# Optimization experiments

Measured on AMD Instinct MI355X. Metric: run time of the kernel, lower is better.

The kernel has to match this reference:

```python
import jax, jax.numpy as jnp
import numpy as np

EPS = 1e-6

def _layernorm2d(x, w, b):
    # normalize over channel dim (axis=1) per (b,h,w)
    u = jnp.mean(x, axis=1, keepdims=True)
    s = jnp.mean((x - u) ** 2, axis=1, keepdims=True)
    xn = (x - u) / jnp.sqrt(s + EPS)
    return xn * w[None, :, None, None] + b[None, :, None, None]

def _conv1x1(x, w, b):
    # w: (O, C, 1, 1)
    y = jnp.einsum('bchw,oc->bohw', x, w[:, :, 0, 0])
    return y + b[None, :, None, None]

def _dwconv3x3(x, w):
    # w: (C, 1, 3, 3), groups = C, padding 1, no bias
    C = x.shape[1]
    return jax.lax.conv_general_dilated(
        x, w, window_strides=(1, 1), padding=((1, 1), (1, 1)),
        dimension_numbers=('NCHW', 'OIHW', 'NCHW'), feature_group_count=C)

def _linrec_scan(a, u, axis):
    # s_t = a_t * s_{t-1} + u_t via associative scan
    def comb(l, r):
        al, ul = l
        ar, ur = r
        return al * ar, ar * ul + ur
    return jax.lax.associative_scan(comb, (a, u), axis=axis)[1]

def _bidir_scan(z, a, b, g, axis):
    u = b * z
    s_f = _linrec_scan(a, u, axis)
    s_b = jnp.flip(_linrec_scan(jnp.flip(a, axis), jnp.flip(u, axis), axis), axis)
    return g * (s_f + s_b)

def setup_inputs() -> dict:
    key = jax.random.key(0)
    ks = jax.random.split(key, 6)
    B, C, H, W = 8, 192, 128, 128
    x = jax.random.normal(ks[0], (B, C, H, W), dtype=jnp.float32)
    ln_w = jnp.ones((C,), jnp.float32)
    ln_b = jnp.zeros((C,), jnp.float32)
    dw_w = jax.random.normal(ks[1], (C, 1, 3, 3), jnp.float32) * (1.0 / 3.0)
    loc_w = jax.random.normal(ks[2], (C, C, 1, 1), jnp.float32) * (1.0 / np.sqrt(C))
    loc_b = jnp.zeros((C,), jnp.float32)
    par_w = jax.random.normal(ks[3], (3 * C, C, 1, 1), jnp.float32) * (1.0 / np.sqrt(C))
    par_b = jnp.zeros((3 * C,), jnp.float32)
    out_w = jax.random.normal(ks[4], (C, C, 1, 1), jnp.float32) * (1.0 / np.sqrt(C))
    out_b = jnp.zeros((C,), jnp.float32)
    return {"x": x, "ln_w": ln_w, "ln_b": ln_b, "dw_w": dw_w,
            "loc_w": loc_w, "loc_b": loc_b, "par_w": par_w, "par_b": par_b,
            "out_w": out_w, "out_b": out_b}

def reference(x, ln_w, ln_b, dw_w, loc_w, loc_b, par_w, par_b, out_w, out_b):
    C = x.shape[1]
    z = _layernorm2d(x, ln_w, ln_b)
    local_feat = _conv1x1(_dwconv3x3(z, dw_w), loc_w, loc_b)
    gates = _conv1x1(z, par_w, par_b)
    alpha = jax.nn.sigmoid(gates[:, :C])
    beta = jax.nn.sigmoid(gates[:, C:2 * C])
    gamma = jax.nn.sigmoid(gates[:, 2 * C:])
    y_w = _bidir_scan(z, alpha, beta, gamma, axis=3)  # along W
    y_h = _bidir_scan(z, alpha, beta, gamma, axis=2)  # along H
    y = local_feat + 0.5 * (y_w + y_h)
    y = jax.nn.silu(y)
    y = _conv1x1(y, out_w, out_b)
    return x + y
```

## Files before the change

### kernel.cpp

```cpp
#include <hip/hip_runtime.h>
#include <cstdint>
#include <cstddef>

#define B 8
#define C 192
#define H 128
#define W 128
#define HW (H * W)
#define CHW ((size_t)C * HW)
#define K C

typedef __attribute__((ext_vector_type(8))) short short8v;
typedef __attribute__((ext_vector_type(4))) float f32x4;
typedef __attribute__((ext_vector_type(4))) unsigned short ushort4v;

__device__ __forceinline__ float bf2f(unsigned short s) {
    union { float f; unsigned u; } cv; cv.u = ((unsigned)s) << 16; return cv.f;
}
__device__ __forceinline__ unsigned short f2bf(float f) {
    union { float f; unsigned u; } cv; cv.f = f;
    unsigned r = (cv.u + 0x7fffu + ((cv.u >> 16) & 1u)) >> 16;
    return (unsigned short)r;
}

__global__ void prepack_kernel(const float* __restrict__ pw, const float* __restrict__ lw,
                               const float* __restrict__ ow, unsigned short* __restrict__ wb) {
    int i = blockIdx.x * 256 + threadIdx.x;
    const int NPW = 3 * C * K, NL = C * K;
    if (i < NPW) wb[i] = f2bf(pw[i]);
    else if (i < NPW + NL) wb[i] = f2bf(lw[i - NPW]);
    else if (i < NPW + 2 * NL) wb[i] = f2bf(ow[i - NPW - NL]);
}

__global__ void ln_kernel(const float* __restrict__ x, const float* __restrict__ lw,
                          const float* __restrict__ lb, unsigned short* __restrict__ zt) {
    int p = blockIdx.x * 256 + threadIdx.x;
    int b = p >> 14, hw = p & 16383;
    const float* xp = x + (size_t)b * CHW + hw;
    float sum = 0.f, sq = 0.f;
    for (int c = 0; c < C; ++c) {
        float v = xp[(size_t)c * HW];
        sum += v; sq += v * v;
    }
    float mean = sum * (1.0f / C);
    float var = fmaxf(sq * (1.0f / C) - mean * mean, 0.f);
    float rs = rsqrtf(var + 1e-6f);
    unsigned short* zp = zt + (size_t)p * K;
#pragma unroll 4
    for (int c8 = 0; c8 < K / 8; ++c8) {
        short8v v;
#pragma unroll
        for (int j = 0; j < 8; ++j) {
            int c = c8 * 8 + j;
            float r = (xp[(size_t)c * HW] - mean) * rs * lw[c] + lb[c];
            v[j] = (short)f2bf(r);
        }
        *(short8v*)(zp + c8 * 8) = v;
    }
}

template <int MODE>
__global__ __launch_bounds__(256, 2)
void conv_mfma_kernel(const unsigned short* __restrict__ zt, const unsigned short* __restrict__ yin,
                      const unsigned short* __restrict__ wb, const float* __restrict__ bias,
                      const float* __restrict__ xres, float* __restrict__ Pf,
                      unsigned short* __restrict__ PA, unsigned short* __restrict__ PU,
                      unsigned short* __restrict__ PG) {
    extern __shared__ char smem[];
    int tid = threadIdx.x;
    int lane = tid & 63, wv = tid >> 6;
    int p0 = blockIdx.x * 256 + wv * 64;
    int lr = lane & 15, lh = lane >> 4;
    int sw = (lr & 7) << 4;

    short8v bfr[4][6];
    if (MODE != 2) {
#pragma unroll
        for (int s = 0; s < 4; ++s) {
            const unsigned short* zr = zt + (size_t)(p0 + s * 16 + lr) * K + lh * 8;
#pragma unroll
            for (int t = 0; t < 6; ++t) bfr[s][t] = *(const short8v*)(zr + t * 32);
        }
    } else {
        int bl = p0 >> 14, hwb = p0 & 16383;
        const unsigned short* yb = yin + (size_t)bl * CHW;
#pragma unroll
        for (int s = 0; s < 4; ++s) {
            int hw = hwb + s * 16 + lr;
#pragma unroll
            for (int t = 0; t < 6; ++t) {
                int c0 = t * 32 + lh * 8;
                short8v v;
#pragma unroll
                for (int j = 0; j < 8; ++j)
                    v[j] = (short)yb[(size_t)(c0 + j) * HW + hw];
                bfr[s][t] = v;
            }
        }
    }

    const int NGY = (MODE == 0) ? 3 : 1;
    for (int gy = 0; gy < NGY; ++gy) {
        if (gy) __syncthreads();
        const unsigned short* wsrc = wb + (size_t)gy * C * K;
#pragma unroll
        for (int it = 0; it < 18; ++it) {
            int e8 = it * 256 + tid;
            int row = e8 / 24;
            int cb = (e8 % 24) * 16;
            short8v v = *(const short8v*)(wsrc + e8 * 8);
            *(short8v*)(smem + row * 384 + (cb ^ ((row & 7) << 4))) = v;
        }
        __syncthreads();

        for (int ot = 0; ot < 12; ++ot) {
            int row = ot * 16 + lr;
            int rb = row * 384;
            f32x4 acc[4];
#pragma unroll
            for (int s = 0; s < 4; ++s) acc[s] = (f32x4){0.f, 0.f, 0.f, 0.f};
#pragma unroll
            for (int t = 0; t < 6; ++t) {
                short8v af = *(const short8v*)(smem + rb + ((t * 64 + lh * 16) ^ sw));
#pragma unroll
                for (int s = 0; s < 4; ++s)
                    acc[s] = __builtin_amdgcn_mfma_f32_16x16x32_bf16(bfr[s][t], af, acc[s], 0, 0, 0);
            }
            int o = row;
            float bi = bias[(MODE == 0 ? gy * C : 0) + o];
#pragma unroll
            for (int s = 0; s < 4; ++s) {
                int pst = p0 + s * 16 + lh * 4;
                int bl = pst >> 14, hw = pst & 16383;
                if (MODE == 0) {
                    ushort4v q;
#pragma unroll
                    for (int j = 0; j < 4; ++j) {
                        float v = acc[s][j] + bi;
                        v = 1.f / (1.f + __expf(-v));
                        if (gy == 1) v *= bf2f(zt[(size_t)(pst + j) * K + o]);
                        q[j] = f2bf(v);
                    }
                    unsigned short* dst = (gy == 0) ? PA : ((gy == 1) ? PU : PG);
                    *(ushort4v*)(dst + (size_t)bl * CHW + (size_t)o * HW + hw) = q;
                } else if (MODE == 1) {
                    ushort4v q;
#pragma unroll
                    for (int j = 0; j < 4; ++j) q[j] = f2bf(acc[s][j] + bi);
                    *(ushort4v*)(PA + (size_t)bl * CHW + (size_t)o * HW + hw) = q;
                } else {
                    size_t ad = (size_t)bl * CHW + (size_t)o * HW + hw;
                    f32x4 x4 = *(const f32x4*)(xres + ad);
                    f32x4 q;
#pragma unroll
                    for (int j = 0; j < 4; ++j) q[j] = acc[s][j] + bi + x4[j];
                    *(f32x4*)(Pf + ad) = q;
                }
            }
        }
    }
}

#define TROWS 180
#define LPAD  392
__global__ __launch_bounds__(256, 2)
void dw3x3_kernel(const unsigned short* __restrict__ zt, const float* __restrict__ wgt,
                  unsigned short* __restrict__ dt) {
    __shared__ char lds[TROWS * LPAD];
    int tid = threadIdx.x;
    int bx = blockIdx.x;
    int bimg = bx >> 7;
    int rem = bx & 127;
    int th = rem >> 3, tw = rem & 7;
    int h0 = th * 8, w0 = tw * 16;
    size_t ibase = (size_t)bimg * HW;

    for (int e = tid; e < TROWS * 24; e += 256) {
        int row = e / 24, ch = e % 24;
        int hh = row / 18, ww = row % 18;
        int h = h0 - 1 + hh, w = w0 - 1 + ww;
        short8v v;
        if (h >= 0 && h < H && w >= 0 && w < W)
            v = *(const short8v*)(zt + (ibase + h * W + w) * K + ch * 8);
        else
            v = (short8v){0, 0, 0, 0, 0, 0, 0, 0};
        *(short8v*)(lds + row * LPAD + ch * 16) = v;
    }
    __syncthreads();

    int w_l = tid & 15, h_l = (tid >> 4) & 7, half = tid >> 7;
    int p_out = (h0 + h_l) * W + (w0 + w_l);
    unsigned short* dp = dt + (ibase + p_out) * K + half * 96;
#pragma unroll
    for (int cc = 0; cc < 12; ++cc) {
        int c8 = half * 12 + cc;
        float acc[8];
#pragma unroll
        for (int j = 0; j < 8; ++j) acc[j] = 0.f;
#pragma unroll
        for (int dy = -1; dy <= 1; ++dy) {
#pragma unroll
            for (int dx = -1; dx <= 1; ++dx) {
                int row = (h_l + 1 + dy) * 18 + (w_l + 1 + dx);
                short8v zv = *(const short8v*)(lds + row * LPAD + c8 * 16);
                int t = (dy + 1) * 3 + (dx + 1);
#pragma unroll
                for (int j = 0; j < 8; ++j)
                    acc[j] += wgt[(c8 * 8 + j) * 9 + t] * bf2f((unsigned short)zv[j]);
            }
        }
        short8v ov;
#pragma unroll
        for (int j = 0; j < 8; ++j) ov[j] = (short)f2bf(acc[j]);
        *(short8v*)(dp + cc * 8) = ov;
    }
}

__global__ __launch_bounds__(1024)
void scan_fused_kernel(const unsigned short* __restrict__ A_, const unsigned short* __restrict__ U_,
                       const unsigned short* __restrict__ G_, unsigned short* __restrict__ LY) {
    extern __shared__ float Sl[];
    float* AF = Sl + HW;
    float* UF = AF + 1024;
    float* AB = UF + 1024;
    float* UB = AB + 1024;
    int tid = threadIdx.x, lane = tid & 63, wvi = tid >> 6;
    size_t pb = (size_t)blockIdx.x * HW;

#pragma unroll
    for (int i = 0; i < 8; ++i) {
        int r = wvi * 8 + i;
        size_t base = pb + (size_t)r * W;
        ushort2 av = *(const ushort2*)(A_ + base + 2 * lane);
        ushort2 uv = *(const ushort2*)(U_ + base + 2 * lane);
        float a0 = bf2f(av.x), a1 = bf2f(av.y);
        float u0 = bf2f(uv.x), u1 = bf2f(uv.y);

        float Aa = a0 * a1;
        float Uu = a1 * u0 + u1;
#pragma unroll
        for (int d = 1; d < 64; d <<= 1) {
            float Ao = __shfl_up(Aa, (unsigned)d, 64);
            float Uo = __shfl_up(Uu, (unsigned)d, 64);
            if (lane >= d) { Uu = Aa * Uo + Uu; Aa = Aa * Ao; }
        }
        float sp = __shfl_up(Uu, 1u, 64);
        if (lane == 0) sp = 0.f;
        float s0 = a0 * sp + u0;
        float s1 = a1 * s0 + u1;

        Aa = a0 * a1;
        Uu = a0 * u1 + u0;
#pragma unroll
        for (int d = 1; d < 64; d <<= 1) {
            float Ao = __shfl_down(Aa, (unsigned)d, 64);
            float Uo = __shfl_down(Uu, (unsigned)d, 64);
            if (lane + d < 64) { Uu = Aa * Uo + Uu; Aa = Aa * Ao; }
        }
        float tn = __shfl_down(Uu, 1u, 64);
        if (lane == 63) tn = 0.f;
        float t1 = a1 * tn + u1;
        float t0 = a0 * t1 + u0;

        Sl[r * W + 2 * lane]     = s0 + t0;
        Sl[r * W + 2 * lane + 1] = s1 + t1;
    }

    int w = tid & 127, ck = tid >> 7;
    int h0 = ck * 16;
    float av[16], uv[16];
#pragma unroll
    for (int i = 0; i < 16; ++i) {
        size_t off = pb + (size_t)(h0 + i) * W + w;
        av[i] = bf2f(A_[off]);
        uv[i] = bf2f(U_[off]);
    }
    float Af = 1.f, Uf = 0.f, Ab = 1.f, Ub = 0.f;
#pragma unroll
    for (int i = 0; i < 16; ++i) { Uf = av[i] * Uf + uv[i]; Af *= av[i]; }
#pragma unroll
    for (int i = 15; i >= 0; --i) { Ub = av[i] * Ub + uv[i]; Ab *= av[i]; }
    AF[ck * 128 + w] = Af; UF[ck * 128 + w] = Uf;
    AB[ck * 128 + w] = Ab; UB[ck * 128 + w] = Ub;
    __syncthreads();

    if (tid < 128) {
        float s = 0.f;
#pragma unroll
        for (int k = 0; k < 8; ++k) {
            float Aa = AF[k * 128 + tid], Uu = UF[k * 128 + tid];
            UF[k * 128 + tid] = s;
            s = Aa * s + Uu;
        }
    } else if (tid < 256) {
        int ww = tid - 128;
        float s = 0.f;
#pragma unroll
        for (int k = 7; k >= 0; --k) {
            float Aa = AB[k * 128 + ww], Uu = UB[k * 128 + ww];
            UB[k * 128 + ww] = s;
            s = Aa * s + Uu;
        }
    }
    __syncthreads();

    float sf = UF[ck * 128 + w];
    float sfa[16];
#pragma unroll
    for (int i = 0; i < 16; ++i) { sf = av[i] * sf + uv[i]; sfa[i] = sf; }
    float sb = UB[ck * 128 + w];
#pragma unroll
    for (int i = 15; i >= 0; --i) {
        sb = av[i] * sb + uv[i];
        size_t off = pb + (size_t)(h0 + i) * W + w;
        float g = bf2f(G_[off]);
        float v = bf2f(LY[off]) + 0.5f * g * (Sl[(h0 + i) * W + w] + sfa[i] + sb);
        LY[off] = f2bf(v / (1.f + __expf(-v)));
    }
}

extern "C" void kernel_launch(void* const* d_in, const int* in_sizes, int n_in,
                              void* d_out, int out_size, void* d_ws, size_t ws_size,
                              hipStream_t stream) {
    const float* x     = (const float*)d_in[0];
    const float* ln_w  = (const float*)d_in[1];
    const float* ln_b  = (const float*)d_in[2];
    const float* dw_w  = (const float*)d_in[3];
    const float* loc_w = (const float*)d_in[4];
    const float* loc_b = (const float*)d_in[5];
    const float* par_w = (const float*)d_in[6];
    const float* par_b = (const float*)d_in[7];
    const float* out_w = (const float*)d_in[8];
    const float* out_b = (const float*)d_in[9];
    float* out = (float*)d_out;
    unsigned short* wsu = (unsigned short*)d_ws;

    const int WBN = 5 * C * K;
    int nb = 8;
    while (nb > 1) {
        size_t need = (size_t)WBN * 2 + (size_t)5 * nb * CHW * 2;
        if (need <= ws_size) break;
        nb >>= 1;
    }

    prepack_kernel<<<(WBN + 255) / 256, 256, 0, stream>>>(par_w, loc_w, out_w, wsu);

    for (int b0 = 0; b0 < B; b0 += nb) {
        size_t ge = (size_t)nb * CHW;
        unsigned short* WB = wsu;
        unsigned short* Ab = wsu + WBN;
        unsigned short* Ub = Ab + ge;
        unsigned short* Gb = Ub + ge;
        unsigned short* ZT = Gb + ge;
        unsigned short* DT = ZT + ge;
        const float* xg = x + (size_t)b0 * CHW;
        int npg = nb * HW;

        ln_kernel<<<npg / 256, 256, 0, stream>>>(xg, ln_w, ln_b, ZT);
        conv_mfma_kernel<0><<<npg / 256, 256, 73728, stream>>>(
            ZT, nullptr, WB, par_b, nullptr, nullptr, Ab, Ub, Gb);
        dw3x3_kernel<<<nb * 128, 256, 0, stream>>>(ZT, dw_w, DT);
        conv_mfma_kernel<1><<<npg / 256, 256, 73728, stream>>>(
            DT, nullptr, WB + 3 * C * K, loc_b, nullptr, nullptr, ZT, nullptr, nullptr);
        scan_fused_kernel<<<nb * C, 1024, (HW + 4096) * 4, stream>>>(Ab, Ub, Gb, ZT);
        conv_mfma_kernel<2><<<npg / 256, 256, 73728, stream>>>(
            nullptr, ZT, WB + 4 * C * K, out_b, xg, out + (size_t)b0 * CHW,
            nullptr, nullptr, nullptr);
    }
}
```

Measured before the change: 382.8 us.

## Halve conv tile and weight LDS staging for higher occupancy; add NCHW z copy

The 1x1 conv MFMA kernel now handles 128 pixels per block instead of 256 and stages weights into LDS in two 96-row halves. This shrinks LDS from 72KB to 36KB and raises launch bounds to 4 blocks per CU for more occupancy. The layernorm kernel also writes a second channel-major copy of z into the DT buffer, so the beta*z gating reads coalesced ushort4 data instead of strided per-element loads. The cost is an extra full z write from LN, twice as many weight reloads (once per half per block), and an extra sync per half.

```diff
diff --git a/kernel.cpp b/kernel.cpp
--- a/kernel.cpp
+++ b/kernel.cpp
@@ -33,7 +33,8 @@
 }
 
 __global__ void ln_kernel(const float* __restrict__ x, const float* __restrict__ lw,
-                          const float* __restrict__ lb, unsigned short* __restrict__ zt) {
+                          const float* __restrict__ lb, unsigned short* __restrict__ zt,
+                          unsigned short* __restrict__ zn) {
     int p = blockIdx.x * 256 + threadIdx.x;
     int b = p >> 14, hw = p & 16383;
     const float* xp = x + (size_t)b * CHW + hw;
@@ -46,6 +47,7 @@
     float var = fmaxf(sq * (1.0f / C) - mean * mean, 0.f);
     float rs = rsqrtf(var + 1e-6f);
     unsigned short* zp = zt + (size_t)p * K;
+    unsigned short* znp = zn + (size_t)b * CHW + hw;
 #pragma unroll 4
     for (int c8 = 0; c8 < K / 8; ++c8) {
         short8v v;
@@ -53,30 +55,33 @@
         for (int j = 0; j < 8; ++j) {
             int c = c8 * 8 + j;
             float r = (xp[(size_t)c * HW] - mean) * rs * lw[c] + lb[c];
-            v[j] = (short)f2bf(r);
+            unsigned short rb = f2bf(r);
+            v[j] = (short)rb;
+            znp[(size_t)c * HW] = rb;
         }
         *(short8v*)(zp + c8 * 8) = v;
     }
 }
 
 template <int MODE>
-__global__ __launch_bounds__(256, 2)
+__global__ __launch_bounds__(256, 4)
 void conv_mfma_kernel(const unsigned short* __restrict__ zt, const unsigned short* __restrict__ yin,
+                      const unsigned short* __restrict__ zn,
                       const unsigned short* __restrict__ wb, const float* __restrict__ bias,
                       const float* __restrict__ xres, float* __restrict__ Pf,
                       unsigned short* __restrict__ PA, unsigned short* __restrict__ PU,
                       unsigned short* __restrict__ PG) {
-    extern __shared__ char smem[];
+    __shared__ char smem[96 * 384];
     int tid = threadIdx.x;
     int lane = tid & 63, wv = tid >> 6;
-    int p0 = blockIdx.x * 256 + wv * 64;
+    int p0 = blockIdx.x * 128 + wv * 32;
     int lr = lane & 15, lh = lane >> 4;
     int sw = (lr & 7) << 4;
 
-    short8v bfr[4][6];
+    short8v bfr[2][6];
     if (MODE != 2) {
 #pragma unroll
-        for (int s = 0; s < 4; ++s) {
+        for (int s = 0; s < 2; ++s) {
             const unsigned short* zr = zt + (size_t)(p0 + s * 16 + lr) * K + lh * 8;
 #pragma unroll
             for (int t = 0; t < 6; ++t) bfr[s][t] = *(const short8v*)(zr + t * 32);
@@ -85,7 +90,7 @@
         int bl = p0 >> 14, hwb = p0 & 16383;
         const unsigned short* yb = yin + (size_t)bl * CHW;
 #pragma unroll
-        for (int s = 0; s < 4; ++s) {
+        for (int s = 0; s < 2; ++s) {
             int hw = hwb + s * 16 + lr;
 #pragma unroll
             for (int t = 0; t < 6; ++t) {
@@ -101,60 +106,65 @@
 
     const int NGY = (MODE == 0) ? 3 : 1;
     for (int gy = 0; gy < NGY; ++gy) {
-        if (gy) __syncthreads();
-        const unsigned short* wsrc = wb + (size_t)gy * C * K;
-#pragma unroll
-        for (int it = 0; it < 18; ++it) {
-            int e8 = it * 256 + tid;
-            int row = e8 / 24;
-            int cb = (e8 % 24) * 16;
-            short8v v = *(const short8v*)(wsrc + e8 * 8);
-            *(short8v*)(smem + row * 384 + (cb ^ ((row & 7) << 4))) = v;
-        }
-        __syncthreads();
-
-        for (int ot = 0; ot < 12; ++ot) {
-            int row = ot * 16 + lr;
-            int rb = row * 384;
-            f32x4 acc[4];
-#pragma unroll
-            for (int s = 0; s < 4; ++s) acc[s] = (f32x4){0.f, 0.f, 0.f, 0.f};
-#pragma unroll
-            for (int t = 0; t < 6; ++t) {
-                short8v af = *(const short8v*)(smem + rb + ((t * 64 + lh * 16) ^ sw));
-#pragma unroll
-                for (int s = 0; s < 4; ++s)
-                    acc[s] = __builtin_amdgcn_mfma_f32_16x16x32_bf16(bfr[s][t], af, acc[s], 0, 0, 0);
+        for (int hf = 0; hf < 2; ++hf) {
+            __syncthreads();
+            const unsigned short* wsrc = wb + (size_t)gy * C * K + (size_t)hf * 96 * K;
+#pragma unroll
+            for (int it = 0; it < 9; ++it) {
+                int e8 = it * 256 + tid;
+                int row = e8 / 24;
+                int cb = (e8 % 24) * 16;
+                short8v v = *(const short8v*)(wsrc + e8 * 8);
+                *(short8v*)(smem + row * 384 + (cb ^ ((row & 7) << 4))) = v;
             }
-            int o = row;
-            float bi = bias[(MODE == 0 ? gy * C : 0) + o];
-#pragma unroll
-            for (int s = 0; s < 4; ++s) {
-                int pst = p0 + s * 16 + lh * 4;
-                int bl = pst >> 14, hw = pst & 16383;
-                if (MODE == 0) {
-                    ushort4v q;
-#pragma unroll
-                    for (int j = 0; j < 4; ++j) {
-                        float v = acc[s][j] + bi;
-                        v = 1.f / (1.f + __expf(-v));
-                        if (gy == 1) v *= bf2f(zt[(size_t)(pst + j) * K + o]);
-                        q[j] = f2bf(v);
+            __syncthreads();
+
+            for (int otl = 0; otl < 6; ++otl) {
+                int ot = hf * 6 + otl;
+                int rb = (otl * 16 + lr) * 384;
+                int o = ot * 16 + lr;
+                f32x4 acc[2];
+#pragma unroll
+                for (int s = 0; s < 2; ++s) acc[s] = (f32x4){0.f, 0.f, 0.f, 0.f};
+#pragma unroll
+                for (int t = 0; t < 6; ++t) {
+                    short8v af = *(const short8v*)(smem + rb + ((t * 64 + lh * 16) ^ sw));
+#pragma unroll
+                    for (int s = 0; s < 2; ++s)
+                        acc[s] = __builtin_amdgcn_mfma_f32_16x16x32_bf16(bfr[s][t], af, acc[s], 0, 0, 0);
+                }
+                float bi = bias[(MODE == 0 ? gy * C : 0) + o];
+#pragma unroll
+                for (int s = 0; s < 2; ++s) {
+                    int pst = p0 + s * 16 + lh * 4;
+                    int bl = pst >> 14, hw = pst & 16383;
+                    if (MODE == 0) {
+                        ushort4v q;
+                        ushort4v z4;
+                        if (gy == 1)
+                            z4 = *(const ushort4v*)(zn + (size_t)bl * CHW + (size_t)o * HW + hw);
+#pragma unroll
+                        for (int j = 0; j < 4; ++j) {
+                            float v = acc[s][j] + bi;
+                            v = 1.f / (1.f + __expf(-v));
+                            if (gy == 1) v *= bf2f(z4[j]);
+                            q[j] = f2bf(v);
+                        }
+                        unsigned short* dst = (gy == 0) ? PA : ((gy == 1) ? PU : PG);
+                        *(ushort4v*)(dst + (size_t)bl * CHW + (size_t)o * HW + hw) = q;
+                    } else if (MODE == 1) {
+                        ushort4v q;
+#pragma unroll
+                        for (int j = 0; j < 4; ++j) q[j] = f2bf(acc[s][j] + bi);
+                        *(ushort4v*)(PA + (size_t)bl * CHW + (size_t)o * HW + hw) = q;
+                    } else {
+                        size_t ad = (size_t)bl * CHW + (size_t)o * HW + hw;
+                        f32x4 x4 = *(const f32x4*)(xres + ad);
+                        f32x4 q;
+#pragma unroll
+                        for (int j = 0; j < 4; ++j) q[j] = acc[s][j] + bi + x4[j];
+                        *(f32x4*)(Pf + ad) = q;
                     }
-                    unsigned short* dst = (gy == 0) ? PA : ((gy == 1) ? PU : PG);
-                    *(ushort4v*)(dst + (size_t)bl * CHW + (size_t)o * HW + hw) = q;
-                } else if (MODE == 1) {
-                    ushort4v q;
-#pragma unroll
-                    for (int j = 0; j < 4; ++j) q[j] = f2bf(acc[s][j] + bi);
-                    *(ushort4v*)(PA + (size_t)bl * CHW + (size_t)o * HW + hw) = q;
-                } else {
-                    size_t ad = (size_t)bl * CHW + (size_t)o * HW + hw;
-                    f32x4 x4 = *(const f32x4*)(xres + ad);
-                    f32x4 q;
-#pragma unroll
-                    for (int j = 0; j < 4; ++j) q[j] = acc[s][j] + bi + x4[j];
-                    *(f32x4*)(Pf + ad) = q;
                 }
             }
         }
@@ -356,15 +366,15 @@
         const float* xg = x + (size_t)b0 * CHW;
         int npg = nb * HW;
 
-        ln_kernel<<<npg / 256, 256, 0, stream>>>(xg, ln_w, ln_b, ZT);
-        conv_mfma_kernel<0><<<npg / 256, 256, 73728, stream>>>(
-            ZT, nullptr, WB, par_b, nullptr, nullptr, Ab, Ub, Gb);
+        ln_kernel<<<npg / 256, 256, 0, stream>>>(xg, ln_w, ln_b, ZT, DT);
+        conv_mfma_kernel<0><<<npg / 128, 256, 0, stream>>>(
+            ZT, nullptr, DT, WB, par_b, nullptr, nullptr, Ab, Ub, Gb);
         dw3x3_kernel<<<nb * 128, 256, 0, stream>>>(ZT, dw_w, DT);
-        conv_mfma_kernel<1><<<npg / 256, 256, 73728, stream>>>(
-            DT, nullptr, WB + 3 * C * K, loc_b, nullptr, nullptr, ZT, nullptr, nullptr);
+        conv_mfma_kernel<1><<<npg / 128, 256, 0, stream>>>(
+            DT, nullptr, nullptr, WB + 3 * C * K, loc_b, nullptr, nullptr, ZT, nullptr, nullptr);
         scan_fused_kernel<<<nb * C, 1024, (HW + 4096) * 4, stream>>>(Ab, Ub, Gb, ZT);
-        conv_mfma_kernel<2><<<npg / 256, 256, 73728, stream>>>(
-            nullptr, ZT, WB + 4 * C * K, out_b, xg, out + (size_t)b0 * CHW,
+        conv_mfma_kernel<2><<<npg / 128, 256, 0, stream>>>(
+            nullptr, ZT, nullptr, WB + 4 * C * K, out_b, xg, out + (size_t)b0 * CHW,
             nullptr, nullptr, nullptr);
     }
 }
```

Result: no change. 385.8 us (+0.8%).
